# Kernel tuning notes

Measured on AMD Instinct MI355X. Metric: run time of the kernel, lower is better.

## Reference

```python
import jax, jax.numpy as jnp
import numpy as np

B, C_IN, N = 64, 64, 4097          # N = T + 1 (index 0 is the null node)
T = N - 1
HID, LAT = 128, 64
EPS = 1e-5


def _tree_conv(trees, children, W, b):
    # trees: (B, C, N); children: (B, 3T) int indices into node axis
    Bn, C, _ = trees.shape
    idx = jnp.broadcast_to(children[:, None, :], (Bn, C, children.shape[1]))
    g = jnp.take_along_axis(trees, idx, axis=2)        # (B, C, 3T) gather
    g = g.reshape(Bn, C, -1, 3)                        # (B, C, T, 3)
    out = jnp.einsum('bctk,ock->bot', g, W) + b[None, :, None]  # (B, O, T)
    zero = jnp.zeros((Bn, out.shape[1], 1), out.dtype)  # null-node column
    return jnp.concatenate([zero, out], axis=2)         # (B, O, T+1)


def _tree_layer_norm(x):
    # normalize over (channels, nodes) per example; torch.std -> ddof=1
    mean = jnp.mean(x, axis=(1, 2), keepdims=True)
    std = jnp.std(x, axis=(1, 2), ddof=1, keepdims=True)
    return (x - mean) / (std + EPS)


def _encode(feats, children, W1, b1, W2, b2):
    x = _tree_conv(feats, children, W1, b1)
    x = jax.nn.relu(_tree_layer_norm(x))
    x = _tree_conv(x, children, W2, b2)
    x = jax.nn.relu(_tree_layer_norm(x))   # dropout is identity in eval
    return jnp.max(x, axis=2)              # DynamicPooling: (B, HID)


def setup_inputs() -> dict:
    key = jax.random.key(0)
    ks = jax.random.split(key, 12)
    s_in = 1.0 / np.sqrt(3 * C_IN)
    s_h = 1.0 / np.sqrt(3 * HID)
    s_fc = 1.0 / np.sqrt(2 * HID)
    return {
        'logical_feats': jax.random.normal(ks[0], (B, C_IN, N), jnp.float32),
        'physical_feats': jax.random.normal(ks[1], (B, C_IN, N), jnp.float32),
        'children': jax.random.randint(ks[2], (B, 3 * T), 0, N, jnp.int32),
        'Wl1': jax.random.normal(ks[3], (HID, C_IN, 3), jnp.float32) * s_in,
        'bl1': jnp.zeros((HID,), jnp.float32),
        'Wl2': jax.random.normal(ks[4], (HID, HID, 3), jnp.float32) * s_h,
        'bl2': jnp.zeros((HID,), jnp.float32),
        'Wp1': jax.random.normal(ks[5], (HID, C_IN, 3), jnp.float32) * s_in,
        'bp1': jnp.zeros((HID,), jnp.float32),
        'Wp2': jax.random.normal(ks[6], (HID, HID, 3), jnp.float32) * s_h,
        'bp2': jnp.zeros((HID,), jnp.float32),
        'Wmu': jax.random.normal(ks[7], (LAT, 2 * HID), jnp.float32) * s_fc,
        'bmu': jnp.zeros((LAT,), jnp.float32),
        'Wlv': jax.random.normal(ks[8], (LAT, 2 * HID), jnp.float32) * s_fc,
        'blv': jnp.zeros((LAT,), jnp.float32),
    }


def reference(logical_feats, physical_feats, children,
              Wl1, bl1, Wl2, bl2, Wp1, bp1, Wp2, bp2,
              Wmu, bmu, Wlv, blv):
    # NOTE: source module passes log_children to BOTH encoders; kept faithful.
    l_embed = _encode(logical_feats, children, Wl1, bl1, Wl2, bl2)
    p_embed = _encode(physical_feats, children, Wp1, bp1, Wp2, bp2)
    combined = jnp.concatenate([l_embed, p_embed], axis=-1)  # (B, 2*HID)
    mu = combined @ Wmu.T + bmu
    logvar = combined @ Wlv.T + blv
    return mu, logvar
```

## Files before the change

kernel.cpp:

```cpp
#include <hip/hip_runtime.h>
#include <hip/hip_bf16.h>

#define NODES 4097
#define TT 4096
#define CIN 64
#define HID 128
#define BATCH 64
#define EPS 1e-5f

typedef short bf16x8 __attribute__((ext_vector_type(8)));
typedef float f32x16 __attribute__((ext_vector_type(16)));

__device__ __forceinline__ void load_lds16(const void* g, void* l) {
    __builtin_amdgcn_global_load_lds(
        (const __attribute__((address_space(1))) unsigned int*)(uintptr_t)g,
        (__attribute__((address_space(3))) unsigned int*)(uintptr_t)l,
        16, 0, 0);
}

__global__ __launch_bounds__(256) void k_transpose(const float* __restrict__ f0,
                                                   const float* __restrict__ f1,
                                                   __hip_bfloat16* __restrict__ out) {
    __shared__ float tile[32][33];
    int z = blockIdx.z;
    int enc = z >> 6, b = z & 63;
    const float* in = enc ? f1 : f0;
    __hip_bfloat16* o = out + (size_t)enc * BATCH * NODES * CIN;
    int n0 = blockIdx.x * 32;
    int c0 = blockIdx.y * 32;
    int tx = threadIdx.x, ty = threadIdx.y;
    for (int i = 0; i < 32; i += 8) {
        int n = n0 + tx, c = c0 + ty + i;
        float v = 0.f;
        if (n < NODES) v = in[((size_t)b * CIN + c) * NODES + n];
        tile[ty + i][tx] = v;
    }
    __syncthreads();
    for (int i = 0; i < 32; i += 8) {
        int n = n0 + ty + i, c = c0 + tx;
        if (n < NODES) o[((size_t)b * NODES + n) * CIN + c] = __float2bfloat16(tile[tx][ty + i]);
    }
}

__global__ void k_wprep(const float* __restrict__ W0, const float* __restrict__ W1,
                        __hip_bfloat16* __restrict__ Wp, int C) {
    int enc = blockIdx.y;
    const float* W = enc ? W1 : W0;
    __hip_bfloat16* o = Wp + (size_t)enc * 3 * C * HID;
    int id = blockIdx.x * 256 + threadIdx.x;
    int total = 3 * C * HID / 8;
    if (id >= total) return;
    int lane = id & 63;
    int ct = (id >> 6) & 3;
    int ks = id >> 8;
    int n = ct * 32 + (lane & 31);
    int kb = ks * 16 + (lane >> 5) * 8;
    union { int4 i; __hip_bfloat16 h[8]; } u;
#pragma unroll
    for (int j = 0; j < 8; ++j) {
        int k = kb + j;
        int slot = k / C, c = k % C;
        u.h[j] = __float2bfloat16(W[(n * C + c) * 3 + slot]);
    }
    ((int4*)o)[id] = u.i;
}

template <int C, bool POOL>
__global__ __launch_bounds__(256) void k_conv_mfma(
    const __hip_bfloat16* __restrict__ xT,
    const int* __restrict__ children,
    const __hip_bfloat16* __restrict__ Wp,
    const float* __restrict__ bias0, const float* __restrict__ bias1,
    __hip_bfloat16* __restrict__ y,
    float* __restrict__ sums,
    float* __restrict__ pool_part) {
    constexpr int KSc = C / 16;
    constexpr int KS = 3 * KSc;
    constexpr int PK = 12;
    constexpr int PH = KS / PK;
    int L = blockIdx.x;
    int xcd = L & 7;
    int idx = L >> 3;
    int xt = idx & 31;
    int bg = (idx >> 5) & 7;
    int enc = idx >> 8;
    int b = xcd + 8 * bg;
    const int t0 = xt * 128;
    const int tid = threadIdx.x;
    const int lane = tid & 63;
    const int w = tid >> 6;
    const int hi = lane >> 5;

    __shared__ __align__(16) int4 B_lds[PK * 4 * 64];

    const __hip_bfloat16* x = xT + (size_t)enc * BATCH * NODES * C;
    const int4* WpB = (const int4*)(Wp + (size_t)enc * 3 * C * HID);
    const float* bias = enc ? bias1 : bias0;
    const int sb = enc * BATCH + b;
    const size_t rowbase = (size_t)b * NODES;
    const long cb3 = (long)b * (3 * TT);
    const int tnode = t0 + w * 32 + (lane & 31);

    const int4* ap[3];
#pragma unroll
    for (int s = 0; s < 3; ++s) {
        int child = children[cb3 + (long)tnode * 3 + s];
        ap[s] = (const int4*)(x + (rowbase + child) * C) + hi;
    }

    f32x16 acc[4] = {};
#pragma unroll
    for (int ph = 0; ph < PH; ++ph) {
        if (ph) __syncthreads();
#pragma unroll
        for (int i = 0; i < PK; ++i) {
            int chunk = w * PK + i;
            load_lds16(WpB + (size_t)(ph * PK * 4 + chunk) * 64 + lane, B_lds + chunk * 64);
        }
        int4 areg[PK];
#pragma unroll
        for (int kk = 0; kk < PK; ++kk) {
            int ksg = ph * PK + kk;
            areg[kk] = ap[ksg / KSc][(ksg % KSc) * 2];
        }
        __syncthreads();
#pragma unroll
        for (int kk = 0; kk < PK; ++kk) {
            union { int4 i; bf16x8 v; } a;
            a.i = areg[kk];
#pragma unroll
            for (int cti = 0; cti < 4; ++cti) {
                union { int4 i; bf16x8 v; } bb;
                bb.i = B_lds[(kk * 4 + cti) * 64 + lane];
                acc[cti] = __builtin_amdgcn_mfma_f32_32x32x16_bf16(a.v, bb.v, acc[cti], 0, 0, 0);
            }
        }
    }

    __syncthreads();
    float* red = (float*)B_lds;
    float* pm = red + 512;
    float bsum = 0.f, bss = 0.f;
    __hip_bfloat16* yp = POOL ? nullptr : (y + (size_t)enc * BATCH * NODES * HID);
    const int rbase = t0 + w * 32 + 4 * hi + 1;
#pragma unroll
    for (int cti = 0; cti < 4; ++cti) {
        int o = cti * 32 + (lane & 31);
        float bv = bias[o];
        f32x16 a = acc[cti];
        float lmax = -3.4e38f;
#pragma unroll
        for (int reg = 0; reg < 16; ++reg) {
            float v = a[reg] + bv;
            bsum += v;
            bss += v * v;
            if (POOL) {
                lmax = fmaxf(lmax, v);
            } else {
                int row = rbase + (reg & 3) + 8 * (reg >> 2);
                yp[(rowbase + row) * HID + o] = __float2bfloat16(v);
            }
        }
        if (POOL) pm[(w * 2 + hi) * 128 + o] = lmax;
    }
    if (!POOL && xt == 0 && tid < HID)
        yp[rowbase * HID + tid] = __float2bfloat16(0.f);

    red[tid] = bsum;
    red[256 + tid] = bss;
    __syncthreads();
    for (int s2 = 128; s2 > 0; s2 >>= 1) {
        if (tid < s2) { red[tid] += red[tid + s2]; red[256 + tid] += red[256 + tid + s2]; }
        __syncthreads();
    }
    if (tid == 0) {
        atomicAdd(&sums[sb * 2], red[0]);
        atomicAdd(&sums[sb * 2 + 1], red[256]);
    }
    if (POOL && tid < HID) {
        float m = -3.4e38f;
#pragma unroll
        for (int s2 = 0; s2 < 8; ++s2) m = fmaxf(m, pm[s2 * 128 + tid]);
        pool_part[((size_t)sb * 32 + xt) * HID + tid] = m;
    }
}

__global__ void k_stats(const float* __restrict__ sums, float* __restrict__ ms) {
    int s = threadIdx.x;
    const float M = (float)HID * (float)NODES;
    float S = sums[s * 2], SS = sums[s * 2 + 1];
    float mean = S / M;
    float var = (SS - S * S / M) / (M - 1.f);
    float sd = sqrtf(fmaxf(var, 0.f));
    ms[s * 2] = mean;
    ms[s * 2 + 1] = 1.f / (sd + EPS);
}

__global__ __launch_bounds__(256) void k_norm(__hip_bfloat16* __restrict__ y,
                                              const float* __restrict__ ms) {
    constexpr int Q = NODES * HID / 8;
    int s = blockIdx.y;
    int q = blockIdx.x * 256 + threadIdx.x;
    if (q >= Q) return;
    float mean = ms[s * 2], scale = ms[s * 2 + 1];
    int4* p = (int4*)(y + (size_t)s * NODES * HID) + q;
    union { int4 i; __hip_bfloat16 h[8]; } u;
    u.i = *p;
#pragma unroll
    for (int j = 0; j < 8; ++j) {
        float f = (__bfloat162float(u.h[j]) - mean) * scale;
        u.h[j] = __float2bfloat16(f > 0.f ? f : 0.f);
    }
    *p = u.i;
}

__global__ __launch_bounds__(128) void k_pool_fin(const float* __restrict__ part,
                                                  const float* __restrict__ ms1,
                                                  float* __restrict__ combined) {
    int b = blockIdx.x, enc = blockIdx.y, o = threadIdx.x;
    int sb = enc * BATCH + b;
    float m = 0.f;
#pragma unroll 4
    for (int s = 0; s < 32; ++s)
        m = fmaxf(m, part[((size_t)sb * 32 + s) * HID + o]);
    float v = (m - ms1[sb * 2]) * ms1[sb * 2 + 1];
    combined[b * 256 + enc * 128 + o] = v > 0.f ? v : 0.f;
}

__global__ __launch_bounds__(128) void k_fc(const float* __restrict__ combined,
                                            const float* __restrict__ Wmu, const float* __restrict__ bmu,
                                            const float* __restrict__ Wlv, const float* __restrict__ blv,
                                            float* __restrict__ out) {
    int b = blockIdx.x;
    int tid = threadIdx.x;
    __shared__ float cb[256];
    cb[tid] = combined[b * 256 + tid];
    cb[tid + 128] = combined[b * 256 + tid + 128];
    __syncthreads();
    const float* W = (tid < 64) ? Wmu : Wlv;
    int l = tid & 63;
    float s = (tid < 64) ? bmu[l] : blv[l];
    for (int j = 0; j < 256; ++j) s += cb[j] * W[l * 256 + j];
    out[(tid < 64 ? 0 : BATCH * 64) + b * 64 + l] = s;
}

extern "C" void kernel_launch(void* const* d_in, const int* in_sizes, int n_in,
                              void* d_out, int out_size, void* d_ws, size_t ws_size,
                              hipStream_t stream) {
    const int* children = (const int*)d_in[2];
    const float* Wmu = (const float*)d_in[11];
    const float* bmu = (const float*)d_in[12];
    const float* Wlv = (const float*)d_in[13];
    const float* blv = (const float*)d_in[14];

    char* ws = (char*)d_ws;
    size_t off = 0;
    auto alloc = [&](size_t bytes) { void* p = ws + off; off += (bytes + 255) & ~(size_t)255; return p; };
    float* sums = (float*)alloc(2 * 2 * BATCH * 2 * sizeof(float));
    float* msbuf = (float*)alloc(2 * 2 * BATCH * 2 * sizeof(float));
    float* combined = (float*)alloc((size_t)BATCH * 256 * sizeof(float));
    float* pool_part = (float*)alloc((size_t)2 * BATCH * 32 * HID * sizeof(float));
    __hip_bfloat16* Wp1 = (__hip_bfloat16*)alloc((size_t)2 * 3 * CIN * HID * sizeof(__hip_bfloat16));
    __hip_bfloat16* Wp2 = (__hip_bfloat16*)alloc((size_t)2 * 3 * HID * HID * sizeof(__hip_bfloat16));
    __hip_bfloat16* fT = (__hip_bfloat16*)alloc((size_t)2 * BATCH * NODES * CIN * sizeof(__hip_bfloat16));
    __hip_bfloat16* y1 = (__hip_bfloat16*)alloc((size_t)2 * BATCH * NODES * HID * sizeof(__hip_bfloat16));

    hipMemsetAsync(sums, 0, 2 * 2 * BATCH * 2 * sizeof(float), stream);

    k_wprep<<<dim3(3 * CIN * HID / 8 / 256, 2), 256, 0, stream>>>(
        (const float*)d_in[3], (const float*)d_in[7], Wp1, CIN);
    k_wprep<<<dim3(3 * HID * HID / 8 / 256, 2), 256, 0, stream>>>(
        (const float*)d_in[5], (const float*)d_in[9], Wp2, HID);
    k_transpose<<<dim3(129, 2, 2 * BATCH), dim3(32, 8), 0, stream>>>(
        (const float*)d_in[0], (const float*)d_in[1], fT);

    k_conv_mfma<CIN, false><<<4096, 256, 0, stream>>>(
        fT, children, Wp1, (const float*)d_in[4], (const float*)d_in[8], y1, sums, nullptr);
    k_stats<<<1, 128, 0, stream>>>(sums, msbuf);
    k_norm<<<dim3((NODES * HID / 8 + 255) / 256, 2 * BATCH), 256, 0, stream>>>(y1, msbuf);
    k_conv_mfma<HID, true><<<4096, 256, 0, stream>>>(
        y1, children, Wp2, (const float*)d_in[6], (const float*)d_in[10], nullptr,
        sums + 256, pool_part);
    k_stats<<<1, 128, 0, stream>>>(sums + 256, msbuf + 256);
    k_pool_fin<<<dim3(BATCH, 2), 128, 0, stream>>>(pool_part, msbuf + 256, combined);

    k_fc<<<BATCH, 128, 0, stream>>>(combined, Wmu, bmu, Wlv, blv, (float*)d_out);
}
```

Measured before the change: 404.2 us.

## Make tree-conv kernels persistent with resident weights and prefetched gathers

The conv kernels now launch 256 blocks of 512 threads instead of 4096 blocks of 256. Each block loads the whole packed weight matrix into LDS once, then loops over 8 node tiles, prefetching the next tile's gathered child rows into registers while the MFMAs for the current tile run. LayerNorm sums and pooling maxima are kept in registers across tiles, so far fewer atomics and pool partials are written, and pool_fin reduces 2 partials instead of 32. In exchange the grid is smaller (256 blocks, about one per CU), LDS use and register pressure grow (all of KS a-fragments are held at once), and there is less latency hiding from having many blocks in flight.

```diff
diff --git a/kernel.cpp b/kernel.cpp
--- a/kernel.cpp
+++ b/kernel.cpp
@@ -66,7 +66,7 @@
 }
 
 template <int C, bool POOL>
-__global__ __launch_bounds__(256) void k_conv_mfma(
+__global__ __launch_bounds__(512, 2) void k_conv_mfma(
     const __hip_bfloat16* __restrict__ xT,
     const int* __restrict__ children,
     const __hip_bfloat16* __restrict__ Wp,
@@ -76,22 +76,23 @@
     float* __restrict__ pool_part) {
     constexpr int KSc = C / 16;
     constexpr int KS = 3 * KSc;
-    constexpr int PK = 12;
-    constexpr int PH = KS / PK;
+    constexpr int CH = KS * 4;
+    constexpr int NT = 8;
+
+    __shared__ __align__(16) int4 B_lds[CH * 64];
+
     int L = blockIdx.x;
     int xcd = L & 7;
     int idx = L >> 3;
-    int xt = idx & 31;
-    int bg = (idx >> 5) & 7;
-    int enc = idx >> 8;
+    int bg = idx & 7;
+    int enc = (idx >> 3) & 1;
+    int half = idx >> 4;
     int b = xcd + 8 * bg;
-    const int t0 = xt * 128;
+
     const int tid = threadIdx.x;
     const int lane = tid & 63;
     const int w = tid >> 6;
     const int hi = lane >> 5;
-
-    __shared__ __align__(16) int4 B_lds[PK * 4 * 64];
 
     const __hip_bfloat16* x = xT + (size_t)enc * BATCH * NODES * C;
     const int4* WpB = (const int4*)(Wp + (size_t)enc * 3 * C * HID);
@@ -99,33 +100,44 @@
     const int sb = enc * BATCH + b;
     const size_t rowbase = (size_t)b * NODES;
     const long cb3 = (long)b * (3 * TT);
-    const int tnode = t0 + w * 32 + (lane & 31);
-
-    const int4* ap[3];
-#pragma unroll
-    for (int s = 0; s < 3; ++s) {
-        int child = children[cb3 + (long)tnode * 3 + s];
-        ap[s] = (const int4*)(x + (rowbase + child) * C) + hi;
-    }
-
-    f32x16 acc[4] = {};
-#pragma unroll
-    for (int ph = 0; ph < PH; ++ph) {
-        if (ph) __syncthreads();
-#pragma unroll
-        for (int i = 0; i < PK; ++i) {
-            int chunk = w * PK + i;
-            load_lds16(WpB + (size_t)(ph * PK * 4 + chunk) * 64 + lane, B_lds + chunk * 64);
+
+#pragma unroll
+    for (int i = 0; i < CH / 8; ++i) {
+        int chunk = w * (CH / 8) + i;
+        load_lds16(WpB + (size_t)chunk * 64 + lane, B_lds + chunk * 64);
+    }
+
+    const int base_node = half * 2048 + w * 32 + (lane & 31);
+    int4 areg[KS];
+    {
+        const int4* ap[3];
+#pragma unroll
+        for (int s = 0; s < 3; ++s) {
+            int child = children[cb3 + (long)base_node * 3 + s];
+            ap[s] = (const int4*)(x + (rowbase + child) * C) + hi;
         }
-        int4 areg[PK];
-#pragma unroll
-        for (int kk = 0; kk < PK; ++kk) {
-            int ksg = ph * PK + kk;
-            areg[kk] = ap[ksg / KSc][(ksg % KSc) * 2];
+#pragma unroll
+        for (int kk = 0; kk < KS; ++kk) areg[kk] = ap[kk / KSc][(kk % KSc) * 2];
+    }
+    __syncthreads();
+
+    float bsum = 0.f, bss = 0.f;
+    float lmax0 = -3.4e38f, lmax1 = -3.4e38f, lmax2 = -3.4e38f, lmax3 = -3.4e38f;
+    __hip_bfloat16* yp = POOL ? nullptr : (y + (size_t)enc * BATCH * NODES * HID);
+
+    for (int t = 0; t < NT; ++t) {
+        const int4* np[3];
+        if (t + 1 < NT) {
+            int tnode = base_node + (t + 1) * 256;
+#pragma unroll
+            for (int s = 0; s < 3; ++s) {
+                int child = children[cb3 + (long)tnode * 3 + s];
+                np[s] = (const int4*)(x + (rowbase + child) * C) + hi;
+            }
         }
-        __syncthreads();
-#pragma unroll
-        for (int kk = 0; kk < PK; ++kk) {
+        f32x16 acc[4] = {};
+#pragma unroll
+        for (int kk = 0; kk < KS; ++kk) {
             union { int4 i; bf16x8 v; } a;
             a.i = areg[kk];
 #pragma unroll
@@ -134,54 +146,65 @@
                 bb.i = B_lds[(kk * 4 + cti) * 64 + lane];
                 acc[cti] = __builtin_amdgcn_mfma_f32_32x32x16_bf16(a.v, bb.v, acc[cti], 0, 0, 0);
             }
+            if (t + 1 < NT) areg[kk] = np[kk / KSc][(kk % KSc) * 2];
         }
-    }
-
-    __syncthreads();
-    float* red = (float*)B_lds;
-    float* pm = red + 512;
-    float bsum = 0.f, bss = 0.f;
-    __hip_bfloat16* yp = POOL ? nullptr : (y + (size_t)enc * BATCH * NODES * HID);
-    const int rbase = t0 + w * 32 + 4 * hi + 1;
-#pragma unroll
-    for (int cti = 0; cti < 4; ++cti) {
-        int o = cti * 32 + (lane & 31);
-        float bv = bias[o];
-        f32x16 a = acc[cti];
-        float lmax = -3.4e38f;
-#pragma unroll
-        for (int reg = 0; reg < 16; ++reg) {
-            float v = a[reg] + bv;
-            bsum += v;
-            bss += v * v;
+        const int rbase = half * 2048 + t * 256 + w * 32 + 4 * hi + 1;
+#pragma unroll
+        for (int cti = 0; cti < 4; ++cti) {
+            int o = cti * 32 + (lane & 31);
+            float bv = bias[o];
+            f32x16 a2 = acc[cti];
+            float lm = -3.4e38f;
+#pragma unroll
+            for (int reg = 0; reg < 16; ++reg) {
+                float v = a2[reg] + bv;
+                bsum += v;
+                bss += v * v;
+                if (POOL) {
+                    lm = fmaxf(lm, v);
+                } else {
+                    int row = rbase + (reg & 3) + 8 * (reg >> 2);
+                    yp[(rowbase + row) * HID + o] = __float2bfloat16(v);
+                }
+            }
             if (POOL) {
-                lmax = fmaxf(lmax, v);
-            } else {
-                int row = rbase + (reg & 3) + 8 * (reg >> 2);
-                yp[(rowbase + row) * HID + o] = __float2bfloat16(v);
+                if (cti == 0) lmax0 = fmaxf(lmax0, lm);
+                else if (cti == 1) lmax1 = fmaxf(lmax1, lm);
+                else if (cti == 2) lmax2 = fmaxf(lmax2, lm);
+                else lmax3 = fmaxf(lmax3, lm);
             }
         }
-        if (POOL) pm[(w * 2 + hi) * 128 + o] = lmax;
-    }
-    if (!POOL && xt == 0 && tid < HID)
+    }
+
+    if (!POOL && half == 0 && tid < HID)
         yp[rowbase * HID + tid] = __float2bfloat16(0.f);
 
+    __syncthreads();
+    float* red = (float*)B_lds;
+    float* pm = red + 1024;
     red[tid] = bsum;
-    red[256 + tid] = bss;
-    __syncthreads();
-    for (int s2 = 128; s2 > 0; s2 >>= 1) {
-        if (tid < s2) { red[tid] += red[tid + s2]; red[256 + tid] += red[256 + tid + s2]; }
+    red[512 + tid] = bss;
+    if (POOL) {
+        int ob = (w * 2 + hi) * 128 + (lane & 31);
+        pm[ob] = lmax0;
+        pm[ob + 32] = lmax1;
+        pm[ob + 64] = lmax2;
+        pm[ob + 96] = lmax3;
+    }
+    __syncthreads();
+    for (int s2 = 256; s2 > 0; s2 >>= 1) {
+        if (tid < s2) { red[tid] += red[tid + s2]; red[512 + tid] += red[512 + tid + s2]; }
         __syncthreads();
     }
     if (tid == 0) {
         atomicAdd(&sums[sb * 2], red[0]);
-        atomicAdd(&sums[sb * 2 + 1], red[256]);
+        atomicAdd(&sums[sb * 2 + 1], red[512]);
     }
     if (POOL && tid < HID) {
         float m = -3.4e38f;
 #pragma unroll
-        for (int s2 = 0; s2 < 8; ++s2) m = fmaxf(m, pm[s2 * 128 + tid]);
-        pool_part[((size_t)sb * 32 + xt) * HID + tid] = m;
+        for (int s2 = 0; s2 < 16; ++s2) m = fmaxf(m, pm[s2 * 128 + tid]);
+        pool_part[((size_t)sb * 2 + half) * HID + tid] = m;
     }
 }
 
@@ -220,9 +243,8 @@
     int b = blockIdx.x, enc = blockIdx.y, o = threadIdx.x;
     int sb = enc * BATCH + b;
     float m = 0.f;
-#pragma unroll 4
-    for (int s = 0; s < 32; ++s)
-        m = fmaxf(m, part[((size_t)sb * 32 + s) * HID + o]);
+    m = fmaxf(m, part[((size_t)sb * 2 + 0) * HID + o]);
+    m = fmaxf(m, part[((size_t)sb * 2 + 1) * HID + o]);
     float v = (m - ms1[sb * 2]) * ms1[sb * 2 + 1];
     combined[b * 256 + enc * 128 + o] = v > 0.f ? v : 0.f;
 }
@@ -259,7 +281,7 @@
     float* sums = (float*)alloc(2 * 2 * BATCH * 2 * sizeof(float));
     float* msbuf = (float*)alloc(2 * 2 * BATCH * 2 * sizeof(float));
     float* combined = (float*)alloc((size_t)BATCH * 256 * sizeof(float));
-    float* pool_part = (float*)alloc((size_t)2 * BATCH * 32 * HID * sizeof(float));
+    float* pool_part = (float*)alloc((size_t)2 * BATCH * 2 * HID * sizeof(float));
     __hip_bfloat16* Wp1 = (__hip_bfloat16*)alloc((size_t)2 * 3 * CIN * HID * sizeof(__hip_bfloat16));
     __hip_bfloat16* Wp2 = (__hip_bfloat16*)alloc((size_t)2 * 3 * HID * HID * sizeof(__hip_bfloat16));
     __hip_bfloat16* fT = (__hip_bfloat16*)alloc((size_t)2 * BATCH * NODES * CIN * sizeof(__hip_bfloat16));
@@ -274,11 +296,11 @@
     k_transpose<<<dim3(129, 2, 2 * BATCH), dim3(32, 8), 0, stream>>>(
         (const float*)d_in[0], (const float*)d_in[1], fT);
 
-    k_conv_mfma<CIN, false><<<4096, 256, 0, stream>>>(
+    k_conv_mfma<CIN, false><<<256, 512, 0, stream>>>(
         fT, children, Wp1, (const float*)d_in[4], (const float*)d_in[8], y1, sums, nullptr);
     k_stats<<<1, 128, 0, stream>>>(sums, msbuf);
     k_norm<<<dim3((NODES * HID / 8 + 255) / 256, 2 * BATCH), 256, 0, stream>>>(y1, msbuf);
-    k_conv_mfma<HID, true><<<4096, 256, 0, stream>>>(
+    k_conv_mfma<HID, true><<<256, 512, 0, stream>>>(
         y1, children, Wp2, (const float*)d_in[6], (const float*)d_in[10], nullptr,
         sums + 256, pool_part);
     k_stats<<<1, 128, 0, stream>>>(sums + 256, msbuf + 256);
```

Result: slower. 785.9 us (+94.5%).
